# Kernel optimization log

Hardware: AMD Instinct MI355X
Metric: run time of the kernel (lower is better)

## Reference

```python
import jax, jax.numpy as jnp
import numpy as np

N_HEADS = 16  # must match init_kwargs
BIAS_SCALE = 0.1


def _src_grid(out_size, in_size):
    # torch F.interpolate bilinear, align_corners=False semantics
    scale = in_size / out_size
    src = jnp.clip((jnp.arange(out_size, dtype=jnp.float32) + 0.5) * scale - 0.5, 0.0)
    i0 = jnp.minimum(jnp.floor(src).astype(jnp.int32), in_size - 1)
    i1 = jnp.minimum(i0 + 1, in_size - 1)
    w = src - i0.astype(jnp.float32)
    return i0, i1, w


def _bilinear_resize(img, out_h, out_w):
    Hin, Win = img.shape[-2], img.shape[-1]
    r0, r1, wy = _src_grid(out_h, Hin)
    c0, c1, wx = _src_grid(out_w, Win)
    rows = img[:, r0, :] * (1.0 - wy)[None, :, None] + img[:, r1, :] * wy[None, :, None]
    return rows[:, :, c0] * (1.0 - wx)[None, None, :] + rows[:, :, c1] * wx[None, None, :]


def setup_inputs() -> dict:
    key = jax.random.key(0)
    ks = jax.random.split(key, 10)
    B, L, D, M, K = 4, 1024, 1024, 64, 32
    s = 0.02
    return {
        "x": jax.random.normal(ks[0], (B, L, D), dtype=jnp.float32),
        "harmonics": jax.random.normal(ks[1], (B, M, K), dtype=jnp.float32),
        "wq": jax.random.normal(ks[2], (D, D), dtype=jnp.float32) * s,
        "bq": jax.random.normal(ks[3], (D,), dtype=jnp.float32) * s,
        "wk": jax.random.normal(ks[4], (D, D), dtype=jnp.float32) * s,
        "bk": jax.random.normal(ks[5], (D,), dtype=jnp.float32) * s,
        "wv": jax.random.normal(ks[6], (D, D), dtype=jnp.float32) * s,
        "bv": jax.random.normal(ks[7], (D,), dtype=jnp.float32) * s,
        "wo": jax.random.normal(ks[8], (D, D), dtype=jnp.float32) * s,
        "bo": jax.random.normal(ks[9], (D,), dtype=jnp.float32) * s,
    }


def reference(x, harmonics, wq, bq, wk, bk, wv, bv, wo, bo):
    B, L, D = x.shape
    hd = D // N_HEADS
    scaling = hd ** -0.5

    def split_heads(t):  # [B, L, D] -> [B, H, L, hd]
        return t.reshape(B, L, N_HEADS, hd).transpose(0, 2, 1, 3)

    q = split_heads(x @ wq.T + bq)
    k = split_heads(x @ wk.T + bk)
    v = split_heads(x @ wv.T + bv)

    scores = jnp.einsum("bhqd,bhkd->bhqk", q, k) * scaling  # [B, H, L, L]

    gram = jnp.einsum("bmk,bnk->bmn", harmonics, harmonics)  # [B, M, M]
    bias = _bilinear_resize(gram, L, L)  # [B, L, L]
    scores = scores + BIAS_SCALE * bias[:, None, :, :]

    attn = jax.nn.softmax(scores, axis=-1)
    out = jnp.einsum("bhqk,bhkd->bhqd", attn, v)  # [B, H, L, hd]
    out = out.transpose(0, 2, 1, 3).reshape(B, L, D)
    return out @ wo.T + bo
```

## Files before the change

### kernel.cpp

```cpp
#include <hip/hip_runtime.h>


using short8  = __attribute__((ext_vector_type(8))) short;
using short4v = __attribute__((ext_vector_type(4))) short;
using float4v = __attribute__((ext_vector_type(4))) float;

#define MFMA16(a, b, c) __builtin_amdgcn_mfma_f32_16x16x32_bf16((a), (b), (c), 0, 0, 0)

#define LOG2E 1.44269504088896f

static __device__ __forceinline__ short f2bf(float f) {
    union { float f; unsigned u; } v; v.f = f;
    unsigned r = v.u + 0x7fffu + ((v.u >> 16) & 1u);
    return (short)(r >> 16);
}

static __device__ __forceinline__ unsigned pack2bf(float lo, float hi) {
    union { float f; unsigned u; } a, b;
    a.f = lo; b.f = hi;
    return __builtin_amdgcn_perm(b.u + 0x8000u, a.u + 0x8000u, 0x07060302u);
}

static __device__ __forceinline__ void dma16(const short* g, short* l) {
    __builtin_amdgcn_global_load_lds((const __attribute__((address_space(1))) void*)g,
                                     (__attribute__((address_space(3))) void*)l, 16, 0, 0);
}

__global__ __launch_bounds__(256) void convert_all(
    const float* __restrict__ x,  const float* __restrict__ wq,
    const float* __restrict__ wk, const float* __restrict__ wv,
    const float* __restrict__ wo, short* __restrict__ xb, short* __restrict__ wb) {
    int idx = blockIdx.x * 256 + threadIdx.x;
    for (int i = idx; i < 2097152; i += gridDim.x * 256) {
        const float* src; short* dst;
        if (i < 1048576) {
            src = x + (size_t)i * 4;
            dst = xb + (size_t)i * 4;
        } else {
            int j = i - 1048576;
            int sel = j >> 18;
            const float* w = (sel == 0) ? wq : (sel == 1) ? wk : (sel == 2) ? wv : wo;
            src = w + (size_t)(j & 262143) * 4;
            dst = wb + (size_t)j * 4;
        }
        float4v v = *(const float4v*)src;
        short4v o;
        o.x = f2bf(v.x); o.y = f2bf(v.y); o.z = f2bf(v.z); o.w = f2bf(v.w);
        *(short4v*)dst = o;
    }
}

__global__ __launch_bounds__(256) void fill_aug(const float* __restrict__ harm,
                                                short* __restrict__ Qp,
                                                short* __restrict__ Kp) {
    int b  = blockIdx.y;
    int lc = blockIdx.x;
    int tid = threadIdx.x;
    int ll = tid >> 3;
    int d8 = (tid & 7) * 8;
    int l  = lc * 32 + ll;

    __shared__ float hs[64][33];
    for (int i = tid; i < 2048; i += 256) hs[i >> 5][i & 31] = harm[(size_t)b * 2048 + i];
    __syncthreads();

    float src = (l + 0.5f) * 0.0625f - 0.5f;
    if (src < 0.f) src = 0.f;
    int r0 = (int)floorf(src); if (r0 > 63) r0 = 63;
    int r1 = r0 + 1;           if (r1 > 63) r1 = 63;
    float wy = src - (float)r0;

    float hr[32];
    #pragma unroll
    for (int k = 0; k < 32; k++) hr[k] = (1.f - wy) * hs[r0][k] + wy * hs[r1][k];

    short8 qa, ka;
    #pragma unroll
    for (int j = 0; j < 8; j++) {
        float g = 0.f;
        #pragma unroll
        for (int k = 0; k < 32; k++) g += hr[k] * hs[d8 + j][k];
        qa[j] = f2bf(0.1f * LOG2E * g);
    }
    #pragma unroll
    for (int j = 0; j < 8; j++) {
        float vv = 0.f;
        if (d8 + j == r0) vv += 1.f - wy;
        if (d8 + j == r1) vv += wy;
        ka[j] = f2bf(vv);
    }
    for (int h = 0; h < 16; h++) {
        size_t base = (((size_t)(b * 16 + h) * 1024 + l) << 7) + 64 + d8;
        *(short8*)(Qp + base) = qa;
        *(short8*)(Kp + base) = ka;
    }
}

template <int MODE>
__global__ __launch_bounds__(256, 2) void gemm_kernel(
    const short* __restrict__ A,
    const short* __restrict__ Wb,
    const float* __restrict__ B0, const float* __restrict__ B1, const float* __restrict__ B2,
    short* __restrict__ Qp, short* __restrict__ Kp, short* __restrict__ Vp,
    float* __restrict__ outF) {
    const int z = blockIdx.z;
    const short* W  = Wb + (size_t)z * 1048576;
    const float* Bs = (z == 0) ? B0 : ((z == 1) ? B1 : B2);

    __shared__ short Sm[2][8192];

    const int tid  = threadIdx.x;
    const int lane = tid & 63;
    const int wv   = tid >> 6;
    const int wm   = (wv >> 1) * 64;
    const int wn   = (wv & 1) * 64;
    const int l16  = lane & 15;
    const int quad = lane >> 4;
    const int bm   = blockIdx.x * 128;
    const int bn   = blockIdx.y * 128;

    const short* aSrc[2];
    const short* wSrc[2];
    #pragma unroll
    for (int j = 0; j < 2; j++) {
        int c = j * 256 + tid;
        int r = c >> 2, gs = (c & 3) ^ ((r >> 1) & 3);
        aSrc[j] = A + (size_t)(bm + r) * 1024 + gs * 8;
        wSrc[j] = W + (size_t)(bn + r) * 1024 + gs * 8;
    }
    const int fr = (quad ^ ((l16 >> 1) & 3)) * 8;
    int ai[4], bi[4];
    #pragma unroll
    for (int t = 0; t < 4; t++) {
        ai[t] = (wm + t * 16 + l16) * 32 + fr;
        bi[t] = 4096 + (wn + t * 16 + l16) * 32 + fr;
    }

    float4v zero4 = {0.f, 0.f, 0.f, 0.f};
    float4v acc[4][4];
    #pragma unroll
    for (int i = 0; i < 4; i++)
        #pragma unroll
        for (int j = 0; j < 4; j++) acc[i][j] = zero4;

    dma16(aSrc[0], &Sm[0][wv * 512]);
    dma16(aSrc[1], &Sm[0][2048 + wv * 512]);
    dma16(wSrc[0], &Sm[0][4096 + wv * 512]);
    dma16(wSrc[1], &Sm[0][6144 + wv * 512]);
    #pragma unroll
    for (int j = 0; j < 2; j++) { aSrc[j] += 32; wSrc[j] += 32; }
    __syncthreads();

    for (int kt = 0; kt < 32; kt++) {
        const int cur = kt & 1, nxt = cur ^ 1;
        if (kt < 31) {
            dma16(aSrc[0], &Sm[nxt][wv * 512]);
            dma16(aSrc[1], &Sm[nxt][2048 + wv * 512]);
            dma16(wSrc[0], &Sm[nxt][4096 + wv * 512]);
            dma16(wSrc[1], &Sm[nxt][6144 + wv * 512]);
            #pragma unroll
            for (int j = 0; j < 2; j++) { aSrc[j] += 32; wSrc[j] += 32; }
        }

        short8 af[4], bfr[4];
        #pragma unroll
        for (int mt = 0; mt < 4; mt++) af[mt]  = *(const short8*)&Sm[cur][ai[mt]];
        #pragma unroll
        for (int nt = 0; nt < 4; nt++) bfr[nt] = *(const short8*)&Sm[cur][bi[nt]];
        #pragma unroll
        for (int mt = 0; mt < 4; mt++)
            #pragma unroll
            for (int nt = 0; nt < 4; nt++)
                acc[mt][nt] = MFMA16(af[mt], bfr[nt], acc[mt][nt]);

        __syncthreads();
    }

    #pragma unroll
    for (int mt = 0; mt < 4; mt++)
        #pragma unroll
        for (int nt = 0; nt < 4; nt++) {
            int col = bn + wn + nt * 16 + l16;
            float bias = Bs[col];
            #pragma unroll
            for (int r = 0; r < 4; r++) {
                int row = bm + wm + mt * 16 + quad * 4 + r;
                float val = acc[mt][nt][r] + bias;
                if (MODE == 1) {
                    outF[(size_t)row * 1024 + col] = val;
                } else {
                    int b = row >> 10, l = row & 1023;
                    int h = col >> 6,  d = col & 63;
                    size_t bhl = (size_t)(b * 16 + h) * 1024 + l;
                    if (z == 0)      Qp[(bhl << 7) + d] = f2bf(val * (0.125f * LOG2E));
                    else if (z == 1) Kp[(bhl << 7) + d] = f2bf(val);
                    else {
                        int slot = (l & ~31) | (((l >> 2) & 3) << 3) |
                                   (((l >> 4) & 1) << 2) | (l & 3);
                        Vp[(((size_t)(b * 16 + h) * 64 + d) << 10) + slot] = f2bf(val);
                    }
                }
            }
        }
}

__global__ __attribute__((amdgpu_flat_work_group_size(256, 256),
                          amdgpu_waves_per_eu(2, 2)))
void flash_kernel(const short* __restrict__ Qp,
                  const short* __restrict__ Kp,
                  const short* __restrict__ Vp,
                  short* __restrict__ AO) {
    const int h  = blockIdx.x;
    const int qb = blockIdx.y;
    const int b  = blockIdx.z;
    const int tid  = threadIdx.x;
    const int lane = tid & 63;
    const int w    = tid >> 6;
    const int l16  = lane & 15;
    const int quad = lane >> 4;
    const size_t bh = (size_t)(b * 16 + h);

    __shared__ short Ks[16384];
    __shared__ short Vs[8192];

    short8 qf[2][4];
    #pragma unroll
    for (int n = 0; n < 2; n++) {
        const short* Qb = Qp + ((bh * 1024 + qb * 128 + w * 32 + n * 16 + l16) << 7) + quad * 8;
        #pragma unroll
        for (int c = 0; c < 4; c++) qf[n][c] = *(const short8*)(Qb + c * 32);
    }

    const short* kSrc[4];
    #pragma unroll
    for (int jj = 0; jj < 4; jj++) {
        int key = (w * 4 + jj) * 4 + quad;
        kSrc[jj] = Kp + (bh << 17) + key * 128 + ((l16 ^ (key & 15)) * 8);
    }
    const short* vSrc[2];
    #pragma unroll
    for (int jj = 0; jj < 2; jj++) {
        int d = (w * 2 + jj) * 8 + (lane >> 3);
        vSrc[jj] = Vp + (bh << 16) + d * 1024 + (((lane & 7) ^ (d & 7)) * 8);
    }

    int krd[4], vrd[2];
    #pragma unroll
    for (int c = 0; c < 4; c++) krd[c] = l16 * 128 + (((c * 4 + quad) ^ l16) * 8);
    #pragma unroll
    for (int g = 0; g < 2; g++) vrd[g] = l16 * 64 + (((g * 4 + quad) ^ (l16 & 7)) * 8);

    #pragma unroll
    for (int jj = 0; jj < 4; jj++) dma16(kSrc[jj], &Ks[w * 2048 + jj * 512]);
    #pragma unroll
    for (int jj = 0; jj < 2; jj++) dma16(vSrc[jj], &Vs[w * 1024 + jj * 512]);
    #pragma unroll
    for (int jj = 0; jj < 4; jj++) kSrc[jj] += 8192;
    #pragma unroll
    for (int jj = 0; jj < 2; jj++) vSrc[jj] += 64;
    int dstK = 8192, dstV = 4096;

    float4v zero4 = {0.f, 0.f, 0.f, 0.f};
    float4v o_acc[4][2];
    #pragma unroll
    for (int mt = 0; mt < 4; mt++)
        #pragma unroll
        for (int n = 0; n < 2; n++) o_acc[mt][n] = zero4;
    float l_part[2] = {0.f, 0.f};

    __syncthreads();

    for (int kt = 0; kt < 16; kt++) {
        if (kt < 15) {
            #pragma unroll
            for (int jj = 0; jj < 4; jj++) dma16(kSrc[jj], &Ks[dstK + w * 2048 + jj * 512]);
            #pragma unroll
            for (int jj = 0; jj < 2; jj++) dma16(vSrc[jj], &Vs[dstV + w * 1024 + jj * 512]);
            #pragma unroll
            for (int jj = 0; jj < 4; jj++) kSrc[jj] += 8192;
            #pragma unroll
            for (int jj = 0; jj < 2; jj++) vSrc[jj] += 64;
            dstK ^= 8192; dstV ^= 4096;
        }

        short8 vf[4][2];
        #pragma unroll
        for (int mt = 0; mt < 4; mt++)
            #pragma unroll
            for (int g = 0; g < 2; g++)
                vf[mt][g] = *(const short8*)&Vs[vrd[g] + mt * 1024];

        float4v s[4][2];
        #pragma unroll
        for (int mt = 0; mt < 4; mt++) {
            short8 kf[4];
            #pragma unroll
            for (int c = 0; c < 4; c++) kf[c] = *(const short8*)&Ks[krd[c] + mt * 2048];
            #pragma unroll
            for (int n = 0; n < 2; n++) {
                s[mt][n] = zero4;
                #pragma unroll
                for (int c = 0; c < 4; c++)
                    s[mt][n] = MFMA16(kf[c], qf[n][c], s[mt][n]);
            }
        }

        #pragma unroll
        for (int mt = 0; mt < 4; mt++)
            #pragma unroll
            for (int n = 0; n < 2; n++)
                #pragma unroll
                for (int r = 0; r < 4; r++) {
                    float p = __builtin_exp2f(s[mt][n][r]);
                    s[mt][n][r] = p;
                    l_part[n] += p;
                }

        #pragma unroll
        for (int g = 0; g < 2; g++) {
            short8 pf[2];
            #pragma unroll
            for (int n = 0; n < 2; n++) {
                union { unsigned u[4]; short8 v; } t;
                t.u[0] = pack2bf(s[2 * g][n][0], s[2 * g][n][1]);
                t.u[1] = pack2bf(s[2 * g][n][2], s[2 * g][n][3]);
                t.u[2] = pack2bf(s[2 * g + 1][n][0], s[2 * g + 1][n][1]);
                t.u[3] = pack2bf(s[2 * g + 1][n][2], s[2 * g + 1][n][3]);
                pf[n] = t.v;
            }
            #pragma unroll
            for (int mt = 0; mt < 4; mt++)
                #pragma unroll
                for (int n = 0; n < 2; n++)
                    o_acc[mt][n] = MFMA16(vf[mt][g], pf[n], o_acc[mt][n]);
        }

        if (kt < 15) __syncthreads();
        #pragma unroll
        for (int c = 0; c < 4; c++) krd[c] ^= 8192;
        #pragma unroll
        for (int g = 0; g < 2; g++) vrd[g] ^= 4096;
    }

    #pragma unroll
    for (int n = 0; n < 2; n++) {
        float l = l_part[n];
        l += __shfl_xor(l, 16, 64);
        l += __shfl_xor(l, 32, 64);
        float inv = 1.0f / l;
        int row = b * 1024 + qb * 128 + w * 32 + n * 16 + l16;
        #pragma unroll
        for (int mt = 0; mt < 4; mt++) {
            short4v ov;
            #pragma unroll
            for (int r = 0; r < 4; r++) ov[r] = f2bf(o_acc[mt][n][r] * inv);
            *(short4v*)(AO + (size_t)row * 1024 + h * 64 + mt * 16 + quad * 4) = ov;
        }
    }
}

extern "C" void kernel_launch(void* const* d_in, const int* in_sizes, int n_in,
                              void* d_out, int out_size, void* d_ws, size_t ws_size,
                              hipStream_t stream) {
    const float* x    = (const float*)d_in[0];
    const float* harm = (const float*)d_in[1];
    const float* wq   = (const float*)d_in[2];
    const float* bq   = (const float*)d_in[3];
    const float* wk   = (const float*)d_in[4];
    const float* bk   = (const float*)d_in[5];
    const float* wv   = (const float*)d_in[6];
    const float* bv   = (const float*)d_in[7];
    const float* wo   = (const float*)d_in[8];
    const float* bo   = (const float*)d_in[9];
    float* outF = (float*)d_out;

    short* xb   = (short*)d_ws;
    short* Qp   = xb + (size_t)4 * 1048576;
    short* Kp   = Qp + (size_t)8 * 1048576;
    short* Vp   = Kp + (size_t)8 * 1048576;
    short* Wqkv = Vp + (size_t)4 * 1048576;
    short* Wob  = Wqkv + (size_t)3 * 1048576;
    short* AO   = xb;

    convert_all<<<dim3(2048), dim3(256), 0, stream>>>(x, wq, wk, wv, wo, xb, Wqkv);
    gemm_kernel<0><<<dim3(32, 8, 3), dim3(256), 0, stream>>>(
        xb, Wqkv, bq, bk, bv, Qp, Kp, Vp, nullptr);
    fill_aug<<<dim3(32, 4), dim3(256), 0, stream>>>(harm, Qp, Kp);
    flash_kernel<<<dim3(16, 8, 4), dim3(256), 0, stream>>>(Qp, Kp, Vp, AO);
    gemm_kernel<1><<<dim3(32, 8, 1), dim3(256), 0, stream>>>(
        AO, Wob, bo, nullptr, nullptr, nullptr, nullptr, nullptr, outF);
}
```

Before: 194.5 us.

## Use 8 waves per flash block with 16 query rows each

The attention kernel now launches 512 threads per block instead of 256. Each wave handles 16 query rows instead of 32, so the per-wave Q fragments, score tiles and output accumulators are halved. The K/V tile loads are split across eight waves, and V fragments are read from LDS just before each PV MFMA instead of being preloaded. This lowers register pressure and raises the waves-per-EU target so more waves can hide latency, at the cost of reading each K/V LDS tile twice as many times per block.

```diff
diff --git a/kernel.cpp b/kernel.cpp
--- a/kernel.cpp
+++ b/kernel.cpp
@@ -204,8 +204,8 @@
         }
 }
 
-__global__ __attribute__((amdgpu_flat_work_group_size(256, 256),
-                          amdgpu_waves_per_eu(2, 2)))
+__global__ __attribute__((amdgpu_flat_work_group_size(512, 512),
+                          amdgpu_waves_per_eu(4, 4)))
 void flash_kernel(const short* __restrict__ Qp,
                   const short* __restrict__ Kp,
                   const short* __restrict__ Vp,
@@ -223,116 +223,98 @@
     __shared__ short Ks[16384];
     __shared__ short Vs[8192];
 
-    short8 qf[2][4];
-    #pragma unroll
-    for (int n = 0; n < 2; n++) {
-        const short* Qb = Qp + ((bh * 1024 + qb * 128 + w * 32 + n * 16 + l16) << 7) + quad * 8;
-        #pragma unroll
-        for (int c = 0; c < 4; c++) qf[n][c] = *(const short8*)(Qb + c * 32);
-    }
-
-    const short* kSrc[4];
-    #pragma unroll
-    for (int jj = 0; jj < 4; jj++) {
-        int key = (w * 4 + jj) * 4 + quad;
+    short8 qf[4];
+    {
+        const short* Qb = Qp + ((bh * 1024 + qb * 128 + w * 16 + l16) << 7) + quad * 8;
+        #pragma unroll
+        for (int c = 0; c < 4; c++) qf[c] = *(const short8*)(Qb + c * 32);
+    }
+
+    const short* kSrc[2];
+    #pragma unroll
+    for (int jj = 0; jj < 2; jj++) {
+        int key = (w * 2 + jj) * 4 + quad;
         kSrc[jj] = Kp + (bh << 17) + key * 128 + ((l16 ^ (key & 15)) * 8);
     }
-    const short* vSrc[2];
-    #pragma unroll
-    for (int jj = 0; jj < 2; jj++) {
-        int d = (w * 2 + jj) * 8 + (lane >> 3);
-        vSrc[jj] = Vp + (bh << 16) + d * 1024 + (((lane & 7) ^ (d & 7)) * 8);
-    }
-
-    int krd[4], vrd[2];
+    const short* vSrc;
+    {
+        int d = w * 8 + (lane >> 3);
+        vSrc = Vp + (bh << 16) + d * 1024 + (((lane & 7) ^ (d & 7)) * 8);
+    }
+
+    int krd[4];
     #pragma unroll
     for (int c = 0; c < 4; c++) krd[c] = l16 * 128 + (((c * 4 + quad) ^ l16) * 8);
+    int vrd[2];
     #pragma unroll
     for (int g = 0; g < 2; g++) vrd[g] = l16 * 64 + (((g * 4 + quad) ^ (l16 & 7)) * 8);
 
     #pragma unroll
-    for (int jj = 0; jj < 4; jj++) dma16(kSrc[jj], &Ks[w * 2048 + jj * 512]);
-    #pragma unroll
-    for (int jj = 0; jj < 2; jj++) dma16(vSrc[jj], &Vs[w * 1024 + jj * 512]);
-    #pragma unroll
-    for (int jj = 0; jj < 4; jj++) kSrc[jj] += 8192;
-    #pragma unroll
-    for (int jj = 0; jj < 2; jj++) vSrc[jj] += 64;
+    for (int jj = 0; jj < 2; jj++) dma16(kSrc[jj], &Ks[w * 1024 + jj * 512]);
+    dma16(vSrc, &Vs[w * 512]);
+    #pragma unroll
+    for (int jj = 0; jj < 2; jj++) kSrc[jj] += 8192;
+    vSrc += 64;
     int dstK = 8192, dstV = 4096;
 
     float4v zero4 = {0.f, 0.f, 0.f, 0.f};
-    float4v o_acc[4][2];
-    #pragma unroll
-    for (int mt = 0; mt < 4; mt++)
-        #pragma unroll
-        for (int n = 0; n < 2; n++) o_acc[mt][n] = zero4;
-    float l_part[2] = {0.f, 0.f};
+    float4v o_acc[4];
+    #pragma unroll
+    for (int mt = 0; mt < 4; mt++) o_acc[mt] = zero4;
+    float l_part = 0.f;
 
     __syncthreads();
 
     for (int kt = 0; kt < 16; kt++) {
         if (kt < 15) {
             #pragma unroll
-            for (int jj = 0; jj < 4; jj++) dma16(kSrc[jj], &Ks[dstK + w * 2048 + jj * 512]);
-            #pragma unroll
-            for (int jj = 0; jj < 2; jj++) dma16(vSrc[jj], &Vs[dstV + w * 1024 + jj * 512]);
-            #pragma unroll
-            for (int jj = 0; jj < 4; jj++) kSrc[jj] += 8192;
-            #pragma unroll
-            for (int jj = 0; jj < 2; jj++) vSrc[jj] += 64;
+            for (int jj = 0; jj < 2; jj++) dma16(kSrc[jj], &Ks[dstK + w * 1024 + jj * 512]);
+            dma16(vSrc, &Vs[dstV + w * 512]);
+            #pragma unroll
+            for (int jj = 0; jj < 2; jj++) kSrc[jj] += 8192;
+            vSrc += 64;
             dstK ^= 8192; dstV ^= 4096;
         }
 
-        short8 vf[4][2];
-        #pragma unroll
-        for (int mt = 0; mt < 4; mt++)
-            #pragma unroll
-            for (int g = 0; g < 2; g++)
-                vf[mt][g] = *(const short8*)&Vs[vrd[g] + mt * 1024];
-
-        float4v s[4][2];
+        float4v s[4];
         #pragma unroll
         for (int mt = 0; mt < 4; mt++) {
             short8 kf[4];
             #pragma unroll
             for (int c = 0; c < 4; c++) kf[c] = *(const short8*)&Ks[krd[c] + mt * 2048];
-            #pragma unroll
-            for (int n = 0; n < 2; n++) {
-                s[mt][n] = zero4;
-                #pragma unroll
-                for (int c = 0; c < 4; c++)
-                    s[mt][n] = MFMA16(kf[c], qf[n][c], s[mt][n]);
+            s[mt] = zero4;
+            #pragma unroll
+            for (int c = 0; c < 4; c++)
+                s[mt] = MFMA16(kf[c], qf[c], s[mt]);
+        }
+
+        #pragma unroll
+        for (int mt = 0; mt < 4; mt++)
+            #pragma unroll
+            for (int r = 0; r < 4; r++) {
+                float p = __builtin_exp2f(s[mt][r]);
+                s[mt][r] = p;
+                l_part += p;
             }
-        }
-
-        #pragma unroll
-        for (int mt = 0; mt < 4; mt++)
-            #pragma unroll
-            for (int n = 0; n < 2; n++)
-                #pragma unroll
-                for (int r = 0; r < 4; r++) {
-                    float p = __builtin_exp2f(s[mt][n][r]);
-                    s[mt][n][r] = p;
-                    l_part[n] += p;
-                }
 
         #pragma unroll
         for (int g = 0; g < 2; g++) {
-            short8 pf[2];
-            #pragma unroll
-            for (int n = 0; n < 2; n++) {
-                union { unsigned u[4]; short8 v; } t;
-                t.u[0] = pack2bf(s[2 * g][n][0], s[2 * g][n][1]);
-                t.u[1] = pack2bf(s[2 * g][n][2], s[2 * g][n][3]);
-                t.u[2] = pack2bf(s[2 * g + 1][n][0], s[2 * g + 1][n][1]);
-                t.u[3] = pack2bf(s[2 * g + 1][n][2], s[2 * g + 1][n][3]);
-                pf[n] = t.v;
+            short8 pf;
+            #pragma unroll
+            for (int j = 0; j < 4; j++) {
+                ((unsigned*)&pf)[j >> 1] = 0;
             }
-            #pragma unroll
-            for (int mt = 0; mt < 4; mt++)
-                #pragma unroll
-                for (int n = 0; n < 2; n++)
-                    o_acc[mt][n] = MFMA16(vf[mt][g], pf[n], o_acc[mt][n]);
+            union { unsigned u[4]; short8 v; } t;
+            t.u[0] = pack2bf(s[2 * g][0], s[2 * g][1]);
+            t.u[1] = pack2bf(s[2 * g][2], s[2 * g][3]);
+            t.u[2] = pack2bf(s[2 * g + 1][0], s[2 * g + 1][1]);
+            t.u[3] = pack2bf(s[2 * g + 1][2], s[2 * g + 1][3]);
+            pf = t.v;
+            #pragma unroll
+            for (int mt = 0; mt < 4; mt++) {
+                short8 vf = *(const short8*)&Vs[vrd[g] + mt * 1024];
+                o_acc[mt] = MFMA16(vf, pf, o_acc[mt]);
+            }
         }
 
         if (kt < 15) __syncthreads();
@@ -342,18 +324,17 @@
         for (int g = 0; g < 2; g++) vrd[g] ^= 4096;
     }
 
-    #pragma unroll
-    for (int n = 0; n < 2; n++) {
-        float l = l_part[n];
+    {
+        float l = l_part;
         l += __shfl_xor(l, 16, 64);
         l += __shfl_xor(l, 32, 64);
         float inv = 1.0f / l;
-        int row = b * 1024 + qb * 128 + w * 32 + n * 16 + l16;
+        int row = b * 1024 + qb * 128 + w * 16 + l16;
         #pragma unroll
         for (int mt = 0; mt < 4; mt++) {
             short4v ov;
             #pragma unroll
-            for (int r = 0; r < 4; r++) ov[r] = f2bf(o_acc[mt][n][r] * inv);
+            for (int r = 0; r < 4; r++) ov[r] = f2bf(o_acc[mt][r] * inv);
             *(short4v*)(AO + (size_t)row * 1024 + h * 64 + mt * 16 + quad * 4) = ov;
         }
     }
@@ -386,7 +367,7 @@
     gemm_kernel<0><<<dim3(32, 8, 3), dim3(256), 0, stream>>>(
         xb, Wqkv, bq, bk, bv, Qp, Kp, Vp, nullptr);
     fill_aug<<<dim3(32, 4), dim3(256), 0, stream>>>(harm, Qp, Kp);
-    flash_kernel<<<dim3(16, 8, 4), dim3(256), 0, stream>>>(Qp, Kp, Vp, AO);
+    flash_kernel<<<dim3(16, 8, 4), dim3(512), 0, stream>>>(Qp, Kp, Vp, AO);
     gemm_kernel<1><<<dim3(32, 8, 1), dim3(256), 0, stream>>>(
         AO, Wob, bo, nullptr, nullptr, nullptr, nullptr, nullptr, outF);
 }
```

After: 194.1 us. Within noise of the previous version (-0.2%).

## Double flash query tile to 256 rows with 8 waves sharing K/V tiles

Applied to the files above, without the earlier changes.

The flash attention block grows from 4 to 8 waves and covers 256 query rows, so each K/V tile loaded into LDS is reused by twice as many queries. Each thread now issues half as many async global-to-LDS copies per tile. V fragments are read from LDS just before each PV MFMA instead of being preloaded, which cuts register pressure. The grid shrinks to 256 blocks, so there is less parallelism per CU and barriers now span more waves.

```diff
diff --git a/kernel.cpp b/kernel.cpp
--- a/kernel.cpp
+++ b/kernel.cpp
@@ -204,7 +204,7 @@
         }
 }
 
-__global__ __attribute__((amdgpu_flat_work_group_size(256, 256),
+__global__ __attribute__((amdgpu_flat_work_group_size(512, 512),
                           amdgpu_waves_per_eu(2, 2)))
 void flash_kernel(const short* __restrict__ Qp,
                   const short* __restrict__ Kp,
@@ -226,38 +226,36 @@
     short8 qf[2][4];
     #pragma unroll
     for (int n = 0; n < 2; n++) {
-        const short* Qb = Qp + ((bh * 1024 + qb * 128 + w * 32 + n * 16 + l16) << 7) + quad * 8;
+        const short* Qb = Qp + ((bh * 1024 + qb * 256 + w * 32 + n * 16 + l16) << 7) + quad * 8;
         #pragma unroll
         for (int c = 0; c < 4; c++) qf[n][c] = *(const short8*)(Qb + c * 32);
     }
 
-    const short* kSrc[4];
-    #pragma unroll
-    for (int jj = 0; jj < 4; jj++) {
-        int key = (w * 4 + jj) * 4 + quad;
+    const short* kSrc[2];
+    #pragma unroll
+    for (int jj = 0; jj < 2; jj++) {
+        int key = (w * 2 + jj) * 4 + quad;
         kSrc[jj] = Kp + (bh << 17) + key * 128 + ((l16 ^ (key & 15)) * 8);
     }
-    const short* vSrc[2];
-    #pragma unroll
-    for (int jj = 0; jj < 2; jj++) {
-        int d = (w * 2 + jj) * 8 + (lane >> 3);
-        vSrc[jj] = Vp + (bh << 16) + d * 1024 + (((lane & 7) ^ (d & 7)) * 8);
-    }
-
-    int krd[4], vrd[2];
+    const short* vSrc;
+    {
+        int d = w * 8 + (lane >> 3);
+        vSrc = Vp + (bh << 16) + d * 1024 + (((lane & 7) ^ (d & 7)) * 8);
+    }
+
+    int krd[4];
     #pragma unroll
     for (int c = 0; c < 4; c++) krd[c] = l16 * 128 + (((c * 4 + quad) ^ l16) * 8);
+    int vrd[2];
     #pragma unroll
     for (int g = 0; g < 2; g++) vrd[g] = l16 * 64 + (((g * 4 + quad) ^ (l16 & 7)) * 8);
 
     #pragma unroll
-    for (int jj = 0; jj < 4; jj++) dma16(kSrc[jj], &Ks[w * 2048 + jj * 512]);
-    #pragma unroll
-    for (int jj = 0; jj < 2; jj++) dma16(vSrc[jj], &Vs[w * 1024 + jj * 512]);
-    #pragma unroll
-    for (int jj = 0; jj < 4; jj++) kSrc[jj] += 8192;
-    #pragma unroll
-    for (int jj = 0; jj < 2; jj++) vSrc[jj] += 64;
+    for (int jj = 0; jj < 2; jj++) dma16(kSrc[jj], &Ks[w * 1024 + jj * 512]);
+    dma16(vSrc, &Vs[w * 512]);
+    #pragma unroll
+    for (int jj = 0; jj < 2; jj++) kSrc[jj] += 8192;
+    vSrc += 64;
     int dstK = 8192, dstV = 4096;
 
     float4v zero4 = {0.f, 0.f, 0.f, 0.f};
@@ -273,22 +271,13 @@
     for (int kt = 0; kt < 16; kt++) {
         if (kt < 15) {
             #pragma unroll
-            for (int jj = 0; jj < 4; jj++) dma16(kSrc[jj], &Ks[dstK + w * 2048 + jj * 512]);
-            #pragma unroll
-            for (int jj = 0; jj < 2; jj++) dma16(vSrc[jj], &Vs[dstV + w * 1024 + jj * 512]);
-            #pragma unroll
-            for (int jj = 0; jj < 4; jj++) kSrc[jj] += 8192;
-            #pragma unroll
-            for (int jj = 0; jj < 2; jj++) vSrc[jj] += 64;
+            for (int jj = 0; jj < 2; jj++) dma16(kSrc[jj], &Ks[dstK + w * 1024 + jj * 512]);
+            dma16(vSrc, &Vs[dstV + w * 512]);
+            #pragma unroll
+            for (int jj = 0; jj < 2; jj++) kSrc[jj] += 8192;
+            vSrc += 64;
             dstK ^= 8192; dstV ^= 4096;
         }
-
-        short8 vf[4][2];
-        #pragma unroll
-        for (int mt = 0; mt < 4; mt++)
-            #pragma unroll
-            for (int g = 0; g < 2; g++)
-                vf[mt][g] = *(const short8*)&Vs[vrd[g] + mt * 1024];
 
         float4v s[4][2];
         #pragma unroll
@@ -329,10 +318,12 @@
                 pf[n] = t.v;
             }
             #pragma unroll
-            for (int mt = 0; mt < 4; mt++)
+            for (int mt = 0; mt < 4; mt++) {
+                short8 vf = *(const short8*)&Vs[vrd[g] + mt * 1024];
                 #pragma unroll
                 for (int n = 0; n < 2; n++)
-                    o_acc[mt][n] = MFMA16(vf[mt][g], pf[n], o_acc[mt][n]);
+                    o_acc[mt][n] = MFMA16(vf, pf[n], o_acc[mt][n]);
+            }
         }
 
         if (kt < 15) __syncthreads();
@@ -348,7 +339,7 @@
         l += __shfl_xor(l, 16, 64);
         l += __shfl_xor(l, 32, 64);
         float inv = 1.0f / l;
-        int row = b * 1024 + qb * 128 + w * 32 + n * 16 + l16;
+        int row = b * 1024 + qb * 256 + w * 32 + n * 16 + l16;
         #pragma unroll
         for (int mt = 0; mt < 4; mt++) {
             short4v ov;
@@ -386,7 +377,7 @@
     gemm_kernel<0><<<dim3(32, 8, 3), dim3(256), 0, stream>>>(
         xb, Wqkv, bq, bk, bv, Qp, Kp, Vp, nullptr);
     fill_aug<<<dim3(32, 4), dim3(256), 0, stream>>>(harm, Qp, Kp);
-    flash_kernel<<<dim3(16, 8, 4), dim3(256), 0, stream>>>(Qp, Kp, Vp, AO);
+    flash_kernel<<<dim3(16, 4, 4), dim3(512), 0, stream>>>(Qp, Kp, Vp, AO);
     gemm_kernel<1><<<dim3(32, 8, 1), dim3(256), 0, stream>>>(
         AO, Wob, bo, nullptr, nullptr, nullptr, nullptr, nullptr, outF);
 }
```

Result: no change. 195.8 us (+0.6%).
